# Performance work log

Hardware: AMD Instinct MI355X
Metric: run time of the kernel (lower is better)

The kernel has to match this reference:

```python
import jax, jax.numpy as jnp
import numpy as np

N, E, F_IN, NHID, HEADS, NGRAPHS = 50000, 800000, 128, 256, 4, 16
C = NHID // HEADS          # 64 per-head channels
NEG_SLOPE = 0.2            # PyG GATConv default negative_slope


def setup_inputs() -> dict:
    key = jax.random.key(0)
    k = jax.random.split(key, 7)
    x = jax.random.normal(k[0], (N, F_IN), jnp.float32)
    edge_index = jax.random.randint(k[1], (2, E), 0, N)          # [2, E] src/dst
    batch = jnp.sort(jax.random.randint(k[2], (N,), 0, NGRAPHS))  # node -> graph id
    # learned params of GATConv(F_IN, C, heads=HEADS), concat=True
    W = jax.random.normal(k[3], (F_IN, NHID), jnp.float32) / np.sqrt(F_IN)
    att_src = jax.random.normal(k[4], (HEADS, C), jnp.float32) * 0.1
    att_dst = jax.random.normal(k[5], (HEADS, C), jnp.float32) * 0.1
    bias = jax.random.normal(k[6], (NHID,), jnp.float32) * 0.01
    return {"x": x, "edge_index": edge_index, "batch": batch,
            "W": W, "att_src": att_src, "att_dst": att_dst, "bias": bias}


def _segment_softmax(logits, seg, num_segments):
    # softmax over all edges sharing the same destination node
    m = jax.ops.segment_max(logits, seg, num_segments=num_segments)
    m = jnp.where(jnp.isfinite(m), m, jnp.zeros_like(m))  # guard empty segments
    e = jnp.exp(logits - m[seg])
    s = jax.ops.segment_sum(e, seg, num_segments=num_segments)
    return e / (s[seg] + 1e-16)


def reference(x, edge_index, batch, W, att_src, att_dst, bias):
    n = x.shape[0]
    # PyG GATConv adds self-loops by default
    loops = jnp.arange(n, dtype=edge_index.dtype)
    src = jnp.concatenate([edge_index[0], loops])
    dst = jnp.concatenate([edge_index[1], loops])
    xp = (x @ W).reshape(n, HEADS, C)                       # [N, H, C]
    a_src = jnp.einsum('nhc,hc->nh', xp, att_src)           # [N, H]
    a_dst = jnp.einsum('nhc,hc->nh', xp, att_dst)
    logits = jax.nn.leaky_relu(a_src[src] + a_dst[dst], NEG_SLOPE)  # [E+N, H]
    alpha = _segment_softmax(logits, dst, n)
    msg = xp[src] * alpha[:, :, None]                       # [E+N, H, C]
    out = jax.ops.segment_sum(msg, dst, num_segments=n).reshape(n, NHID) + bias
    h = jax.nn.relu(out)                                    # hidden_act='relu'
    # global max / mean pooling per graph, then concat
    gmax = jax.ops.segment_max(h, batch, num_segments=NGRAPHS)
    cnt = jax.ops.segment_sum(jnp.ones((n, 1), h.dtype), batch, num_segments=NGRAPHS)
    gmean = jax.ops.segment_sum(h, batch, num_segments=NGRAPHS) / (cnt + 1e-16)
    return jnp.concatenate([gmax, gmean], axis=1)           # [NGRAPHS, 2*NHID]
```

## Files before the change

kernel.cpp:

```cpp
#include <hip/hip_runtime.h>

#define NN 50000
#define NE 800000
#define FIN 128
#define NHID 256
#define HEADS 4
#define CPH 64
#define NG 16
#define ETOT (NE + NN)
#define NEG_SLOPE 0.2f
#define MAXDEG 64

__device__ __forceinline__ float lrelu(float x) {
    return x > 0.f ? x : NEG_SLOPE * x;
}
__device__ __forceinline__ unsigned short bf16_rne(float f) {
    unsigned u = __float_as_uint(f);
    unsigned r = (u + 0x7fffu + ((u >> 16) & 1u)) >> 16;
    return (unsigned short)r;
}
__device__ __forceinline__ float bf16_to_f(unsigned short h) {
    return __uint_as_float((unsigned)h << 16);
}

using frag_ab = __attribute__((ext_vector_type(8))) short;
using frag_cd = __attribute__((ext_vector_type(4))) float;

__global__ __launch_bounds__(256) void k_prep(const float* __restrict__ W,
                                              unsigned short* __restrict__ Wt16) {
    int idx = blockIdx.x * 256 + threadIdx.x;
    int n = idx >> 7;
    int k = idx & 127;
    Wt16[idx] = bf16_rne(W[(size_t)k * NHID + n]);
}

__global__ __launch_bounds__(256) void k_gemm(const float* __restrict__ x,
                                              const unsigned short* __restrict__ Wt16,
                                              const float* __restrict__ att_src,
                                              const float* __restrict__ att_dst,
                                              unsigned short* __restrict__ xp16,
                                              float* __restrict__ a_src,
                                              float* __restrict__ a_dst) {
    __shared__ __align__(16) unsigned short xs[64][136];
    const int tid = threadIdx.x;
    const int row0 = blockIdx.x * 64;

    {
        int r = tid >> 2;
        int c0 = (tid & 3) * 32;
        int gr = row0 + r;
        if (gr < NN) {
            #pragma unroll
            for (int i = 0; i < 8; i++) {
                float4 v = *(const float4*)&x[(size_t)gr * FIN + c0 + i * 4];
                ushort4 o;
                o.x = bf16_rne(v.x); o.y = bf16_rne(v.y);
                o.z = bf16_rne(v.z); o.w = bf16_rne(v.w);
                *(ushort4*)&xs[r][c0 + i * 4] = o;
            }
        } else {
            ushort4 z = {0, 0, 0, 0};
            #pragma unroll
            for (int i = 0; i < 8; i++) *(ushort4*)&xs[r][c0 + i * 4] = z;
        }
    }
    __syncthreads();

    const int wv = tid >> 6;
    const int lane = tid & 63;
    const int rowhalf = wv >> 1;
    const int colhalf = wv & 1;
    const int m = lane & 15;
    const int q = lane >> 4;
    const int cbase = colhalf * 128;

    frag_cd acc[2][8];
    #pragma unroll
    for (int rt = 0; rt < 2; rt++)
        #pragma unroll
        for (int c = 0; c < 8; c++)
            acc[rt][c] = (frag_cd){0.f, 0.f, 0.f, 0.f};

    #pragma unroll
    for (int k0 = 0; k0 < FIN; k0 += 32) {
        frag_ab af0 = *(const frag_ab*)&xs[rowhalf * 32 + m][k0 + q * 8];
        frag_ab af1 = *(const frag_ab*)&xs[rowhalf * 32 + 16 + m][k0 + q * 8];
        #pragma unroll
        for (int c = 0; c < 8; c++) {
            int n = cbase + c * 16 + m;
            frag_ab bf = *(const frag_ab*)&Wt16[(size_t)n * FIN + k0 + q * 8];
            acc[0][c] = __builtin_amdgcn_mfma_f32_16x16x32_bf16(af0, bf, acc[0][c], 0, 0, 0);
            acc[1][c] = __builtin_amdgcn_mfma_f32_16x16x32_bf16(af1, bf, acc[1][c], 0, 0, 0);
        }
    }

    float asv[8], adv[8];
    #pragma unroll
    for (int c = 0; c < 8; c++) {
        asv[c] = att_src[cbase + c * 16 + m];
        adv[c] = att_dst[cbase + c * 16 + m];
    }
    const int headA = colhalf * 2;
    const int headB = colhalf * 2 + 1;

    #pragma unroll
    for (int rt = 0; rt < 2; rt++) {
        #pragma unroll
        for (int reg = 0; reg < 4; reg++) {
            int grow = row0 + rowhalf * 32 + rt * 16 + q * 4 + reg;
            bool ok = grow < NN;
            if (ok) {
                #pragma unroll
                for (int c = 0; c < 8; c++)
                    xp16[(size_t)grow * NHID + cbase + c * 16 + m] = bf16_rne(acc[rt][c][reg]);
            }
            float psA = 0.f, psB = 0.f, pdA = 0.f, pdB = 0.f;
            #pragma unroll
            for (int c = 0; c < 4; c++) {
                psA += acc[rt][c][reg] * asv[c];
                pdA += acc[rt][c][reg] * adv[c];
                psB += acc[rt][c + 4][reg] * asv[c + 4];
                pdB += acc[rt][c + 4][reg] * adv[c + 4];
            }
            #pragma unroll
            for (int off = 1; off < 16; off <<= 1) {
                psA += __shfl_xor(psA, off, 64);
                psB += __shfl_xor(psB, off, 64);
                pdA += __shfl_xor(pdA, off, 64);
                pdB += __shfl_xor(pdB, off, 64);
            }
            if (m == 0 && ok) {
                a_src[grow * 4 + headA] = psA;
                a_src[grow * 4 + headB] = psB;
                a_dst[grow * 4 + headA] = pdA;
                a_dst[grow * 4 + headB] = pdB;
            }
        }
    }
}

__global__ __launch_bounds__(256) void k_scatter(const int* __restrict__ ei,
                                                 int* __restrict__ deg,
                                                 unsigned short* __restrict__ elist) {
    int e = blockIdx.x * 256 + threadIdx.x;
    if (e >= ETOT) return;
    int s, d;
    if (e < NE) { s = ei[e]; d = ei[NE + e]; } else { s = d = e - NE; }
    int pos = atomicAdd(&deg[d], 1);
    if (pos < MAXDEG) elist[d * MAXDEG + pos] = (unsigned short)s;
}

__global__ __launch_bounds__(256) void k_agg(const unsigned short* __restrict__ elist,
                                             const int* __restrict__ deg,
                                             const float* __restrict__ a_src,
                                             const float* __restrict__ a_dst,
                                             const unsigned short* __restrict__ xp16,
                                             const float* __restrict__ bias,
                                             float* __restrict__ hbuf) {
    __shared__ float wlds[4][MAXDEG][4];
    __shared__ int   slds[4][MAXDEG];
    int wv = threadIdx.x >> 6;
    int lane = threadIdx.x & 63;
    int d = blockIdx.x * 4 + wv;
    if (d >= NN) return;
    int dg = deg[d]; if (dg > MAXDEG) dg = MAXDEG;

    float4 ad = *(const float4*)&a_dst[d * 4];

    float4 lg = make_float4(-1e30f, -1e30f, -1e30f, -1e30f);
    if (lane < dg) {
        int s = elist[d * MAXDEG + lane];
        slds[wv][lane] = s;
        float4 as = *(const float4*)&a_src[s * 4];
        lg.x = lrelu(as.x + ad.x);
        lg.y = lrelu(as.y + ad.y);
        lg.z = lrelu(as.z + ad.z);
        lg.w = lrelu(as.w + ad.w);
    }
    float4 m = lg;
    #pragma unroll
    for (int off = 1; off < 64; off <<= 1) {
        m.x = fmaxf(m.x, __shfl_xor(m.x, off, 64));
        m.y = fmaxf(m.y, __shfl_xor(m.y, off, 64));
        m.z = fmaxf(m.z, __shfl_xor(m.z, off, 64));
        m.w = fmaxf(m.w, __shfl_xor(m.w, off, 64));
    }
    float4 w = make_float4(0.f, 0.f, 0.f, 0.f);
    if (lane < dg) {
        w.x = expf(lg.x - m.x);
        w.y = expf(lg.y - m.y);
        w.z = expf(lg.z - m.z);
        w.w = expf(lg.w - m.w);
    }
    *(float4*)&wlds[wv][lane][0] = w;
    float4 sm = w;
    #pragma unroll
    for (int off = 1; off < 64; off <<= 1) {
        sm.x += __shfl_xor(sm.x, off, 64);
        sm.y += __shfl_xor(sm.y, off, 64);
        sm.z += __shfl_xor(sm.z, off, 64);
        sm.w += __shfl_xor(sm.w, off, 64);
    }
    int h = lane >> 4;
    float denom = (h == 0 ? sm.x : h == 1 ? sm.y : h == 2 ? sm.z : sm.w) + 1e-16f;

    float4 acc0 = make_float4(0.f, 0.f, 0.f, 0.f);
    float4 acc1 = make_float4(0.f, 0.f, 0.f, 0.f);
    float4 acc2 = make_float4(0.f, 0.f, 0.f, 0.f);
    float4 acc3 = make_float4(0.f, 0.f, 0.f, 0.f);
    int e = 0;
    for (; e + 4 <= dg; e += 4) {
        int s0 = slds[wv][e + 0], s1 = slds[wv][e + 1];
        int s2 = slds[wv][e + 2], s3 = slds[wv][e + 3];
        float w0 = wlds[wv][e + 0][h], w1 = wlds[wv][e + 1][h];
        float w2 = wlds[wv][e + 2][h], w3 = wlds[wv][e + 3][h];
        ushort4 v0 = *(const ushort4*)&xp16[(size_t)s0 * NHID + lane * 4];
        ushort4 v1 = *(const ushort4*)&xp16[(size_t)s1 * NHID + lane * 4];
        ushort4 v2 = *(const ushort4*)&xp16[(size_t)s2 * NHID + lane * 4];
        ushort4 v3 = *(const ushort4*)&xp16[(size_t)s3 * NHID + lane * 4];
        acc0.x += w0 * bf16_to_f(v0.x); acc0.y += w0 * bf16_to_f(v0.y);
        acc0.z += w0 * bf16_to_f(v0.z); acc0.w += w0 * bf16_to_f(v0.w);
        acc1.x += w1 * bf16_to_f(v1.x); acc1.y += w1 * bf16_to_f(v1.y);
        acc1.z += w1 * bf16_to_f(v1.z); acc1.w += w1 * bf16_to_f(v1.w);
        acc2.x += w2 * bf16_to_f(v2.x); acc2.y += w2 * bf16_to_f(v2.y);
        acc2.z += w2 * bf16_to_f(v2.z); acc2.w += w2 * bf16_to_f(v2.w);
        acc3.x += w3 * bf16_to_f(v3.x); acc3.y += w3 * bf16_to_f(v3.y);
        acc3.z += w3 * bf16_to_f(v3.z); acc3.w += w3 * bf16_to_f(v3.w);
    }
    for (; e < dg; e++) {
        int s0 = slds[wv][e];
        float w0 = wlds[wv][e][h];
        ushort4 v0 = *(const ushort4*)&xp16[(size_t)s0 * NHID + lane * 4];
        acc0.x += w0 * bf16_to_f(v0.x); acc0.y += w0 * bf16_to_f(v0.y);
        acc0.z += w0 * bf16_to_f(v0.z); acc0.w += w0 * bf16_to_f(v0.w);
    }
    float4 acc;
    acc.x = (acc0.x + acc1.x) + (acc2.x + acc3.x);
    acc.y = (acc0.y + acc1.y) + (acc2.y + acc3.y);
    acc.z = (acc0.z + acc1.z) + (acc2.z + acc3.z);
    acc.w = (acc0.w + acc1.w) + (acc2.w + acc3.w);

    float4 b = *(const float4*)&bias[lane * 4];
    float4 hv;
    hv.x = fmaxf(acc.x / denom + b.x, 0.f);
    hv.y = fmaxf(acc.y / denom + b.y, 0.f);
    hv.z = fmaxf(acc.z / denom + b.z, 0.f);
    hv.w = fmaxf(acc.w / denom + b.w, 0.f);
    *(float4*)&hbuf[(size_t)d * NHID + lane * 4] = hv;
}

#define NPB 128
__global__ __launch_bounds__(256) void k_pool(const float* __restrict__ hbuf,
                                              const int* __restrict__ batch,
                                              float* __restrict__ gmax,
                                              float* __restrict__ gsum) {
    int c = threadIdx.x;
    int n0 = blockIdx.x * NPB;
    if (n0 >= NN) return;
    float lmax = 0.f, lsum = 0.f;
    int cur_g = batch[n0];
    int nend = n0 + NPB; if (nend > NN) nend = NN;
    for (int n = n0; n < nend; n++) {
        int g = batch[n];
        if (g != cur_g) {
            atomicMax((int*)&gmax[cur_g * NHID + c], __float_as_int(lmax));
            atomicAdd(&gsum[cur_g * NHID + c], lsum);
            lmax = 0.f; lsum = 0.f; cur_g = g;
        }
        float val = hbuf[(size_t)n * NHID + c];
        lmax = fmaxf(lmax, val);
        lsum += val;
    }
    atomicMax((int*)&gmax[cur_g * NHID + c], __float_as_int(lmax));
    atomicAdd(&gsum[cur_g * NHID + c], lsum);
}

__device__ __forceinline__ int lb_batch(const int* __restrict__ batch, int val) {
    int lo = 0, hi = NN;
    while (lo < hi) {
        int mid = (lo + hi) >> 1;
        if (batch[mid] < val) lo = mid + 1; else hi = mid;
    }
    return lo;
}

__global__ __launch_bounds__(512) void k_final(const float* __restrict__ gmax,
                                               const float* __restrict__ gsum,
                                               const int* __restrict__ batch,
                                               float* __restrict__ out) {
    __shared__ float inv_cnt;
    int g = blockIdx.x;
    if (threadIdx.x == 0) {
        int lo = lb_batch(batch, g);
        int hi = lb_batch(batch, g + 1);
        inv_cnt = 1.0f / ((float)(hi - lo) + 1e-16f);
    }
    __syncthreads();
    int j = threadIdx.x;
    float v;
    if (j < 256) v = gmax[g * NHID + j];
    else v = gsum[g * NHID + (j - 256)] * inv_cnt;
    out[g * 512 + j] = v;
}

extern "C" void kernel_launch(void* const* d_in, const int* in_sizes, int n_in,
                              void* d_out, int out_size, void* d_ws, size_t ws_size,
                              hipStream_t stream) {
    const float* x      = (const float*)d_in[0];
    const int*   ei     = (const int*)d_in[1];
    const int*   batch  = (const int*)d_in[2];
    const float* W      = (const float*)d_in[3];
    const float* attS   = (const float*)d_in[4];
    const float* attD   = (const float*)d_in[5];
    const float* bias   = (const float*)d_in[6];
    float* out = (float*)d_out;

    float* ws = (float*)d_ws;
    unsigned short* xp16  = (unsigned short*)ws;
    float*          a_src = (float*)(xp16 + (size_t)NN * NHID + 256);
    float*          a_dst = a_src + 200000;
    float*          hbuf  = a_dst + 200000;
    unsigned short* elist = (unsigned short*)(hbuf + 12800000);
    int*            deg   = (int*)(elist + (size_t)NN * MAXDEG);
    float*          gmax  = (float*)(deg + NN);
    float*          gsum  = gmax + 4096;
    unsigned short* Wt16  = (unsigned short*)(gsum + 4096);

    size_t zero_bytes = (size_t)(NN + 4096 + 4096) * 4;
    hipMemsetAsync((void*)deg, 0, zero_bytes, stream);

    k_prep<<<128, 256, 0, stream>>>(W, Wt16);
    k_gemm<<<(NN + 63) / 64, 256, 0, stream>>>(x, Wt16, attS, attD, xp16, a_src, a_dst);
    k_scatter<<<(ETOT + 255) / 256, 256, 0, stream>>>(ei, deg, elist);
    k_agg<<<(NN + 3) / 4, 256, 0, stream>>>(elist, deg, a_src, a_dst, xp16, bias, hbuf);
    k_pool<<<(NN + NPB - 1) / NPB, 256, 0, stream>>>(hbuf, batch, gmax, gsum);
    k_final<<<NG, 512, 0, stream>>>(gmax, gsum, batch, out);
}
```

Baseline: 275.1 us.

## Merge W prep into scatter, stage GEMM output in LDS, prefetch gathers, bf16 hidden buffer

Folds the W transpose/convert kernel into the edge-scatter kernel, which removes one launch. The GEMM now writes its bf16 output through shared memory so the global stores are full 16-byte rows, where before they were scattered 2-byte writes. The aggregation loop software-prefetches the next group of four neighbour rows, and the hidden activations are stored as bf16 rather than fp32, halving the write and the pool read traffic. The cost is a larger LDS footprint in the GEMM, which may lower occupancy, and extra rounding of h before pooling.

```diff
diff --git a/kernel.cpp b/kernel.cpp
--- a/kernel.cpp
+++ b/kernel.cpp
@@ -26,12 +26,25 @@
 using frag_ab = __attribute__((ext_vector_type(8))) short;
 using frag_cd = __attribute__((ext_vector_type(4))) float;
 
-__global__ __launch_bounds__(256) void k_prep(const float* __restrict__ W,
-                                              unsigned short* __restrict__ Wt16) {
-    int idx = blockIdx.x * 256 + threadIdx.x;
-    int n = idx >> 7;
-    int k = idx & 127;
-    Wt16[idx] = bf16_rne(W[(size_t)k * NHID + n]);
+__global__ __launch_bounds__(256) void k_scatter(const int* __restrict__ ei,
+                                                 const float* __restrict__ W,
+                                                 unsigned short* __restrict__ Wt16,
+                                                 int* __restrict__ deg,
+                                                 unsigned short* __restrict__ elist) {
+    int bid = blockIdx.x;
+    if (bid < 128) {
+        int idx = bid * 256 + threadIdx.x;
+        int n = idx >> 7;
+        int k = idx & 127;
+        Wt16[idx] = bf16_rne(W[(size_t)k * NHID + n]);
+        return;
+    }
+    int e = (bid - 128) * 256 + threadIdx.x;
+    if (e >= ETOT) return;
+    int s, d;
+    if (e < NE) { s = ei[e]; d = ei[NE + e]; } else { s = d = e - NE; }
+    int pos = atomicAdd(&deg[d], 1);
+    if (pos < MAXDEG) elist[d * MAXDEG + pos] = (unsigned short)s;
 }
 
 __global__ __launch_bounds__(256) void k_gemm(const float* __restrict__ x,
@@ -41,7 +54,7 @@
                                               unsigned short* __restrict__ xp16,
                                               float* __restrict__ a_src,
                                               float* __restrict__ a_dst) {
-    __shared__ __align__(16) unsigned short xs[64][136];
+    __shared__ __align__(16) unsigned short smem[64 * 264];
     const int tid = threadIdx.x;
     const int row0 = blockIdx.x * 64;
 
@@ -56,12 +69,12 @@
                 ushort4 o;
                 o.x = bf16_rne(v.x); o.y = bf16_rne(v.y);
                 o.z = bf16_rne(v.z); o.w = bf16_rne(v.w);
-                *(ushort4*)&xs[r][c0 + i * 4] = o;
+                *(ushort4*)&smem[r * 264 + c0 + i * 4] = o;
             }
         } else {
             ushort4 z = {0, 0, 0, 0};
             #pragma unroll
-            for (int i = 0; i < 8; i++) *(ushort4*)&xs[r][c0 + i * 4] = z;
+            for (int i = 0; i < 8; i++) *(ushort4*)&smem[r * 264 + c0 + i * 4] = z;
         }
     }
     __syncthreads();
@@ -83,8 +96,8 @@
 
     #pragma unroll
     for (int k0 = 0; k0 < FIN; k0 += 32) {
-        frag_ab af0 = *(const frag_ab*)&xs[rowhalf * 32 + m][k0 + q * 8];
-        frag_ab af1 = *(const frag_ab*)&xs[rowhalf * 32 + 16 + m][k0 + q * 8];
+        frag_ab af0 = *(const frag_ab*)&smem[(rowhalf * 32 + m) * 264 + k0 + q * 8];
+        frag_ab af1 = *(const frag_ab*)&smem[(rowhalf * 32 + 16 + m) * 264 + k0 + q * 8];
         #pragma unroll
         for (int c = 0; c < 8; c++) {
             int n = cbase + c * 16 + m;
@@ -109,11 +122,6 @@
         for (int reg = 0; reg < 4; reg++) {
             int grow = row0 + rowhalf * 32 + rt * 16 + q * 4 + reg;
             bool ok = grow < NN;
-            if (ok) {
-                #pragma unroll
-                for (int c = 0; c < 8; c++)
-                    xp16[(size_t)grow * NHID + cbase + c * 16 + m] = bf16_rne(acc[rt][c][reg]);
-            }
             float psA = 0.f, psB = 0.f, pdA = 0.f, pdB = 0.f;
             #pragma unroll
             for (int c = 0; c < 4; c++) {
@@ -137,17 +145,35 @@
             }
         }
     }
-}
-
-__global__ __launch_bounds__(256) void k_scatter(const int* __restrict__ ei,
-                                                 int* __restrict__ deg,
-                                                 unsigned short* __restrict__ elist) {
-    int e = blockIdx.x * 256 + threadIdx.x;
-    if (e >= ETOT) return;
-    int s, d;
-    if (e < NE) { s = ei[e]; d = ei[NE + e]; } else { s = d = e - NE; }
-    int pos = atomicAdd(&deg[d], 1);
-    if (pos < MAXDEG) elist[d * MAXDEG + pos] = (unsigned short)s;
+
+    __syncthreads();
+    #pragma unroll
+    for (int rt = 0; rt < 2; rt++)
+        #pragma unroll
+        for (int c = 0; c < 8; c++)
+            #pragma unroll
+            for (int reg = 0; reg < 4; reg++)
+                smem[(rowhalf * 32 + rt * 16 + q * 4 + reg) * 264 + cbase + c * 16 + m] =
+                    bf16_rne(acc[rt][c][reg]);
+    __syncthreads();
+    {
+        int r = tid >> 2;
+        int cg = (tid & 3) * 64;
+        int gr = row0 + r;
+        if (gr < NN) {
+            #pragma unroll
+            for (int j = 0; j < 2; j++) {
+                uint4 v0 = *(const uint4*)&smem[r * 264 + cg + j * 32];
+                uint4 v1 = *(const uint4*)&smem[r * 264 + cg + j * 32 + 8];
+                uint4 v2 = *(const uint4*)&smem[r * 264 + cg + j * 32 + 16];
+                uint4 v3 = *(const uint4*)&smem[r * 264 + cg + j * 32 + 24];
+                *(uint4*)&xp16[(size_t)gr * NHID + cg + j * 32] = v0;
+                *(uint4*)&xp16[(size_t)gr * NHID + cg + j * 32 + 8] = v1;
+                *(uint4*)&xp16[(size_t)gr * NHID + cg + j * 32 + 16] = v2;
+                *(uint4*)&xp16[(size_t)gr * NHID + cg + j * 32 + 24] = v3;
+            }
+        }
+    }
 }
 
 __global__ __launch_bounds__(256) void k_agg(const unsigned short* __restrict__ elist,
@@ -156,7 +182,7 @@
                                              const float* __restrict__ a_dst,
                                              const unsigned short* __restrict__ xp16,
                                              const float* __restrict__ bias,
-                                             float* __restrict__ hbuf) {
+                                             unsigned short* __restrict__ hbuf16) {
     __shared__ float wlds[4][MAXDEG][4];
     __shared__ int   slds[4][MAXDEG];
     int wv = threadIdx.x >> 6;
@@ -208,16 +234,32 @@
     float4 acc1 = make_float4(0.f, 0.f, 0.f, 0.f);
     float4 acc2 = make_float4(0.f, 0.f, 0.f, 0.f);
     float4 acc3 = make_float4(0.f, 0.f, 0.f, 0.f);
-    int e = 0;
-    for (; e + 4 <= dg; e += 4) {
-        int s0 = slds[wv][e + 0], s1 = slds[wv][e + 1];
-        int s2 = slds[wv][e + 2], s3 = slds[wv][e + 3];
-        float w0 = wlds[wv][e + 0][h], w1 = wlds[wv][e + 1][h];
-        float w2 = wlds[wv][e + 2][h], w3 = wlds[wv][e + 3][h];
-        ushort4 v0 = *(const ushort4*)&xp16[(size_t)s0 * NHID + lane * 4];
-        ushort4 v1 = *(const ushort4*)&xp16[(size_t)s1 * NHID + lane * 4];
-        ushort4 v2 = *(const ushort4*)&xp16[(size_t)s2 * NHID + lane * 4];
-        ushort4 v3 = *(const ushort4*)&xp16[(size_t)s3 * NHID + lane * 4];
+    int nfull = dg >> 2;
+    ushort4 v0, v1, v2, v3;
+    float w0 = 0.f, w1 = 0.f, w2 = 0.f, w3 = 0.f;
+    if (nfull > 0) {
+        int s0 = slds[wv][0], s1 = slds[wv][1], s2 = slds[wv][2], s3 = slds[wv][3];
+        w0 = wlds[wv][0][h]; w1 = wlds[wv][1][h];
+        w2 = wlds[wv][2][h]; w3 = wlds[wv][3][h];
+        v0 = *(const ushort4*)&xp16[(size_t)s0 * NHID + lane * 4];
+        v1 = *(const ushort4*)&xp16[(size_t)s1 * NHID + lane * 4];
+        v2 = *(const ushort4*)&xp16[(size_t)s2 * NHID + lane * 4];
+        v3 = *(const ushort4*)&xp16[(size_t)s3 * NHID + lane * 4];
+    }
+    for (int g = 0; g < nfull; g++) {
+        ushort4 p0, p1, p2, p3;
+        float pw0 = 0.f, pw1 = 0.f, pw2 = 0.f, pw3 = 0.f;
+        if (g + 1 < nfull) {
+            int eb = (g + 1) * 4;
+            int s0 = slds[wv][eb + 0], s1 = slds[wv][eb + 1];
+            int s2 = slds[wv][eb + 2], s3 = slds[wv][eb + 3];
+            pw0 = wlds[wv][eb + 0][h]; pw1 = wlds[wv][eb + 1][h];
+            pw2 = wlds[wv][eb + 2][h]; pw3 = wlds[wv][eb + 3][h];
+            p0 = *(const ushort4*)&xp16[(size_t)s0 * NHID + lane * 4];
+            p1 = *(const ushort4*)&xp16[(size_t)s1 * NHID + lane * 4];
+            p2 = *(const ushort4*)&xp16[(size_t)s2 * NHID + lane * 4];
+            p3 = *(const ushort4*)&xp16[(size_t)s3 * NHID + lane * 4];
+        }
         acc0.x += w0 * bf16_to_f(v0.x); acc0.y += w0 * bf16_to_f(v0.y);
         acc0.z += w0 * bf16_to_f(v0.z); acc0.w += w0 * bf16_to_f(v0.w);
         acc1.x += w1 * bf16_to_f(v1.x); acc1.y += w1 * bf16_to_f(v1.y);
@@ -226,13 +268,15 @@
         acc2.z += w2 * bf16_to_f(v2.z); acc2.w += w2 * bf16_to_f(v2.w);
         acc3.x += w3 * bf16_to_f(v3.x); acc3.y += w3 * bf16_to_f(v3.y);
         acc3.z += w3 * bf16_to_f(v3.z); acc3.w += w3 * bf16_to_f(v3.w);
-    }
-    for (; e < dg; e++) {
+        v0 = p0; v1 = p1; v2 = p2; v3 = p3;
+        w0 = pw0; w1 = pw1; w2 = pw2; w3 = pw3;
+    }
+    for (int e = nfull * 4; e < dg; e++) {
         int s0 = slds[wv][e];
-        float w0 = wlds[wv][e][h];
-        ushort4 v0 = *(const ushort4*)&xp16[(size_t)s0 * NHID + lane * 4];
-        acc0.x += w0 * bf16_to_f(v0.x); acc0.y += w0 * bf16_to_f(v0.y);
-        acc0.z += w0 * bf16_to_f(v0.z); acc0.w += w0 * bf16_to_f(v0.w);
+        float we = wlds[wv][e][h];
+        ushort4 vv = *(const ushort4*)&xp16[(size_t)s0 * NHID + lane * 4];
+        acc0.x += we * bf16_to_f(vv.x); acc0.y += we * bf16_to_f(vv.y);
+        acc0.z += we * bf16_to_f(vv.z); acc0.w += we * bf16_to_f(vv.w);
     }
     float4 acc;
     acc.x = (acc0.x + acc1.x) + (acc2.x + acc3.x);
@@ -241,16 +285,16 @@
     acc.w = (acc0.w + acc1.w) + (acc2.w + acc3.w);
 
     float4 b = *(const float4*)&bias[lane * 4];
-    float4 hv;
-    hv.x = fmaxf(acc.x / denom + b.x, 0.f);
-    hv.y = fmaxf(acc.y / denom + b.y, 0.f);
-    hv.z = fmaxf(acc.z / denom + b.z, 0.f);
-    hv.w = fmaxf(acc.w / denom + b.w, 0.f);
-    *(float4*)&hbuf[(size_t)d * NHID + lane * 4] = hv;
+    ushort4 o;
+    o.x = bf16_rne(fmaxf(acc.x / denom + b.x, 0.f));
+    o.y = bf16_rne(fmaxf(acc.y / denom + b.y, 0.f));
+    o.z = bf16_rne(fmaxf(acc.z / denom + b.z, 0.f));
+    o.w = bf16_rne(fmaxf(acc.w / denom + b.w, 0.f));
+    *(ushort4*)&hbuf16[(size_t)d * NHID + lane * 4] = o;
 }
 
 #define NPB 128
-__global__ __launch_bounds__(256) void k_pool(const float* __restrict__ hbuf,
+__global__ __launch_bounds__(256) void k_pool(const unsigned short* __restrict__ hbuf16,
                                               const int* __restrict__ batch,
                                               float* __restrict__ gmax,
                                               float* __restrict__ gsum) {
@@ -267,7 +311,7 @@
             atomicAdd(&gsum[cur_g * NHID + c], lsum);
             lmax = 0.f; lsum = 0.f; cur_g = g;
         }
-        float val = hbuf[(size_t)n * NHID + c];
+        float val = bf16_to_f(hbuf16[(size_t)n * NHID + c]);
         lmax = fmaxf(lmax, val);
         lsum += val;
     }
@@ -316,23 +360,22 @@
     float* out = (float*)d_out;
 
     float* ws = (float*)d_ws;
-    unsigned short* xp16  = (unsigned short*)ws;
-    float*          a_src = (float*)(xp16 + (size_t)NN * NHID + 256);
-    float*          a_dst = a_src + 200000;
-    float*          hbuf  = a_dst + 200000;
-    unsigned short* elist = (unsigned short*)(hbuf + 12800000);
-    int*            deg   = (int*)(elist + (size_t)NN * MAXDEG);
-    float*          gmax  = (float*)(deg + NN);
-    float*          gsum  = gmax + 4096;
-    unsigned short* Wt16  = (unsigned short*)(gsum + 4096);
+    unsigned short* xp16   = (unsigned short*)ws;
+    float*          a_src  = (float*)(xp16 + (size_t)NN * NHID + 256);
+    float*          a_dst  = a_src + 200000;
+    unsigned short* hbuf16 = (unsigned short*)(a_dst + 200000);
+    unsigned short* elist  = hbuf16 + (size_t)NN * NHID;
+    int*            deg    = (int*)(elist + (size_t)NN * MAXDEG);
+    float*          gmax   = (float*)(deg + NN);
+    float*          gsum   = gmax + 4096;
+    unsigned short* Wt16   = (unsigned short*)(gsum + 4096);
 
     size_t zero_bytes = (size_t)(NN + 4096 + 4096) * 4;
     hipMemsetAsync((void*)deg, 0, zero_bytes, stream);
 
-    k_prep<<<128, 256, 0, stream>>>(W, Wt16);
+    k_scatter<<<128 + (ETOT + 255) / 256, 256, 0, stream>>>(ei, W, Wt16, deg, elist);
     k_gemm<<<(NN + 63) / 64, 256, 0, stream>>>(x, Wt16, attS, attD, xp16, a_src, a_dst);
-    k_scatter<<<(ETOT + 255) / 256, 256, 0, stream>>>(ei, deg, elist);
-    k_agg<<<(NN + 3) / 4, 256, 0, stream>>>(elist, deg, a_src, a_dst, xp16, bias, hbuf);
-    k_pool<<<(NN + NPB - 1) / NPB, 256, 0, stream>>>(hbuf, batch, gmax, gsum);
+    k_agg<<<(NN + 3) / 4, 256, 0, stream>>>(elist, deg, a_src, a_dst, xp16, bias, hbuf16);
+    k_pool<<<(NN + NPB - 1) / NPB, 256, 0, stream>>>(hbuf16, batch, gmax, gsum);
     k_final<<<NG, 512, 0, stream>>>(gmax, gsum, batch, out);
 }
```

After: 287.0 us. 4.3% more time.
